# Kernel optimization log

Measured on AMD Instinct MI355X. Metric: run time of the kernel, lower is better.

The kernel has to match this reference:

```python
import jax, jax.numpy as jnp
import numpy as np

N_RULES = 4095
N_TAGS = N_RULES + 1
T = 1024
START = 0
NEG = -10000.0


def setup_inputs() -> dict:
    key = jax.random.key(0)
    k1, k2, k3 = jax.random.split(key, 3)
    feats = jax.random.normal(k1, (T, 1, N_RULES), dtype=jnp.float32)
    transitions = jax.random.normal(k2, (N_TAGS, N_TAGS), dtype=jnp.float32)
    transitions = transitions.at[START, :].set(NEG)  # matches nn.Parameter init edit
    tags = jax.random.randint(k3, (T,), 1, N_TAGS, dtype=jnp.int32)  # valid tags are 1..n_tags-1
    return {"feats": feats, "transitions": transitions, "tags": tags}


def reference(feats, transitions, tags):
    feats2 = feats[:, 0, :]  # [T, n_rules]

    # ---- log_cond_prob (score of the given tag path) ----
    tags_full = jnp.concatenate([jnp.array([START], dtype=tags.dtype), tags])  # [T+1]
    prev = tags_full[:-1]  # tags[t]   in torch code
    nxt = tags_full[1:]    # tags[t+1] in torch code
    # torch: feat[0][tags[t]-1]; tags[t]=0 gives index -1 (wraps) -> emulate with modulo
    emit = feats2[jnp.arange(T), (prev - 1) % N_RULES]          # [T]
    trans = transitions[nxt, prev]                               # [T]
    logprob = jnp.sum(emit + trans)

    # ---- log_normalizer (forward algorithm), vectorized over tags, scan over time ----
    init = jnp.full((N_TAGS,), NEG, dtype=feats.dtype).at[START].set(0.0)
    trans_tail = transitions[1:, :]  # [n_rules, n_tags]; row rule+1 of transitions
    neg_head = jnp.full((1,), NEG, dtype=feats.dtype)

    def step(acc, feat_t):
        # scores[rule, j] = acc[j] + feat_t[rule] + transitions[rule+1, j]
        scores = acc[None, :] + feat_t[:, None] + trans_tail     # [n_rules, n_tags]
        new_tail = jax.nn.logsumexp(scores, axis=1)              # [n_rules]
        new_acc = jnp.concatenate([neg_head, new_tail])          # acc[0] stays -10000
        return new_acc, None

    acc, _ = jax.lax.scan(step, init, feats2)
    Z = jax.nn.logsumexp(acc)

    return jnp.reshape(-(logprob - Z), (1,))
```

## Files before the change

kernel.cpp:

```cpp
#include <hip/hip_runtime.h>


#define T_STEPS 1024
#define NRULES  4095
#define NTAGS   4096
#define RING    8
#define L2E     1.4426950408889634f
#define LN2     0.69314718055994530942

__device__ __forceinline__ float ld_agent(const float* p) {
  return __hip_atomic_load(p, __ATOMIC_RELAXED, __HIP_MEMORY_SCOPE_AGENT);
}
__device__ __forceinline__ void st_agent(float* p, float v) {
  __hip_atomic_store(p, v, __ATOMIC_RELAXED, __HIP_MEMORY_SCOPE_AGENT);
}

__global__ void crf_init(float* __restrict__ pring) {
  const float NANF = __builtin_nanf("");
  int idx = blockIdx.x * blockDim.x + threadIdx.x;
  int stride = gridDim.x * blockDim.x;
  for (int i = idx; i < RING * NTAGS; i += stride) {
    int slot = i >> 12;
    float v = (slot == 0) ? ((i == 0) ? 1.0f : 0.0f) : NANF;
    st_agent(&pring[i], v);
  }
}

__global__ void crf_logprob(const float* __restrict__ feats,
                            const float* __restrict__ trans,
                            const int* __restrict__ tags,
                            float* __restrict__ lp) {
  int t = threadIdx.x;
  int prev = (t == 0) ? 0 : tags[t - 1];
  int nxt  = tags[t];
  int er = prev - 1; if (er < 0) er += NRULES;
  float v = feats[(size_t)t * NRULES + er] + trans[(size_t)nxt * NTAGS + prev];
  #pragma unroll
  for (int d = 32; d; d >>= 1) v += __shfl_xor(v, d, 64);
  __shared__ float sb[16];
  if ((t & 63) == 0) sb[t >> 6] = v;
  __syncthreads();
  if (t == 0) {
    float s = 0.f;
    #pragma unroll
    for (int i = 0; i < 16; ++i) s += sb[i];
    lp[0] = s;
  }
}

__launch_bounds__(512, 2)
__global__ void crf_scan(const float* __restrict__ feats,
                         const float* __restrict__ trans,
                         float* __restrict__ pring,
                         const float* __restrict__ lp,
                         float* __restrict__ out)
{
  const int g    = blockIdx.x;
  const int tid  = threadIdx.x;
  const int wave = tid >> 6;
  const int lane = tid & 63;
  const int tagbase = g * 16 + wave * 2;

  __shared__ __align__(16) float stage[4352];
  __shared__ float wmax[8];
  __shared__ int giveup;

  float E0[64], E1[64];
  {
    const float* rp0 = trans + (size_t)(tagbase + 0) * NTAGS + lane * 64;
    const float* rp1 = trans + (size_t)(tagbase + 1) * NTAGS + lane * 64;
#define LDE(R, K) do {                                                  \
    const float4 v_ = *reinterpret_cast<const float4*>(rp##R + 4*(K));  \
    E##R[4*(K)+0] = __builtin_amdgcn_exp2f(v_.x * L2E);                 \
    E##R[4*(K)+1] = __builtin_amdgcn_exp2f(v_.y * L2E);                 \
    E##R[4*(K)+2] = __builtin_amdgcn_exp2f(v_.z * L2E);                 \
    E##R[4*(K)+3] = __builtin_amdgcn_exp2f(v_.w * L2E);                 \
  } while (0)
    LDE(0,0);  LDE(0,1);  LDE(0,2);  LDE(0,3);
    LDE(0,4);  LDE(0,5);  LDE(0,6);  LDE(0,7);
    LDE(0,8);  LDE(0,9);  LDE(0,10); LDE(0,11);
    LDE(0,12); LDE(0,13); LDE(0,14); LDE(0,15);
    LDE(1,0);  LDE(1,1);  LDE(1,2);  LDE(1,3);
    LDE(1,4);  LDE(1,5);  LDE(1,6);  LDE(1,7);
    LDE(1,8);  LDE(1,9);  LDE(1,10); LDE(1,11);
    LDE(1,12); LDE(1,13); LDE(1,14); LDE(1,15);
#undef LDE
  }

  if (tid == 0) giveup = 0;

  double Racc = 0.0;

  for (int t = 1; t <= T_STEPS; ++t) {
    const int sprev = (t - 1) & (RING - 1);
    const int scur  = t & (RING - 1);
    const float* pprev = pring + sprev * NTAGS;

    __syncthreads();

    if (giveup) break;

    float pv[8];
    #pragma unroll
    for (int i = 0; i < 8; ++i) pv[i] = ld_agent(&pprev[tid + 512 * i]);
    {
      int rounds = 0;
      for (;;) {
        bool bad = false;
        #pragma unroll
        for (int i = 0; i < 8; ++i) bad |= (pv[i] != pv[i]);
        if (__ballot(bad) == 0ull) break;
        if (++rounds > (1 << 18)) { giveup = 1; break; }
        __builtin_amdgcn_s_sleep(1);
        #pragma unroll
        for (int i = 0; i < 8; ++i)
          if (pv[i] != pv[i]) pv[i] = ld_agent(&pprev[tid + 512 * i]);
      }
    }

    if (t >= 2 && wave == 0 && lane < 16)
      st_agent(&pring[((t - 2) & (RING - 1)) * NTAGS + g * 16 + lane],
               __builtin_nanf(""));

    float mloc = 0.0f;
    #pragma unroll
    for (int i = 0; i < 8; ++i) {
      const int f = tid + 512 * i;
      stage[f + 4 * (f >> 6)] = pv[i];
      mloc = fmaxf(mloc, pv[i]);
    }
    #pragma unroll
    for (int d = 32; d; d >>= 1) mloc = fmaxf(mloc, __shfl_xor(mloc, d, 64));
    if (lane == 0) wmax[wave] = mloc;

    const int fi0 = (tagbase == 0) ? 0 : tagbase - 1;
    const float fe0 = feats[(size_t)(t - 1) * NRULES + fi0] * L2E;
    const float fe1 = feats[(size_t)(t - 1) * NRULES + tagbase] * L2E;

    __syncthreads();

    if (giveup) break;

    float pmax = wmax[0];
    #pragma unroll
    for (int i = 1; i < 8; ++i) pmax = fmaxf(pmax, wmax[i]);
    const float rprev = __builtin_amdgcn_logf(pmax);
    Racc += (double)rprev;

    float a0 = 0.f, a1 = 0.f;
    const float* myp = stage + 68 * lane;
#define MAC4(K) do {                                                     \
    const float4 q_ = *reinterpret_cast<const float4*>(myp + 4*(K));     \
    a0 = fmaf(E0[4*(K)+0], q_.x, a0); a1 = fmaf(E1[4*(K)+0], q_.x, a1);  \
    a0 = fmaf(E0[4*(K)+1], q_.y, a0); a1 = fmaf(E1[4*(K)+1], q_.y, a1);  \
    a0 = fmaf(E0[4*(K)+2], q_.z, a0); a1 = fmaf(E1[4*(K)+2], q_.z, a1);  \
    a0 = fmaf(E0[4*(K)+3], q_.w, a0); a1 = fmaf(E1[4*(K)+3], q_.w, a1);  \
  } while (0)
    MAC4(0);  MAC4(1);  MAC4(2);  MAC4(3);
    MAC4(4);  MAC4(5);  MAC4(6);  MAC4(7);
    MAC4(8);  MAC4(9);  MAC4(10); MAC4(11);
    MAC4(12); MAC4(13); MAC4(14); MAC4(15);
#undef MAC4
    #pragma unroll
    for (int d = 32; d; d >>= 1) {
      a0 += __shfl_xor(a0, d, 64);
      a1 += __shfl_xor(a1, d, 64);
    }

    const float y0 = fe0 + __builtin_amdgcn_logf(a0) - rprev;
    const float y1 = fe1 + __builtin_amdgcn_logf(a1) - rprev;

    if (lane < 2) {
      const float y = (lane == 0) ? y0 : y1;
      st_agent(&pring[scur * NTAGS + tagbase + lane], __builtin_amdgcn_exp2f(y));
    }
  }

  if (g == 0) {
    const float* pT = pring + (T_STEPS & (RING - 1)) * NTAGS;
    float pv[8];
    #pragma unroll
    for (int i = 0; i < 8; ++i) pv[i] = ld_agent(&pT[tid + 512 * i]);
    {
      int rounds = 0;
      for (;;) {
        bool bad = false;
        #pragma unroll
        for (int i = 0; i < 8; ++i) bad |= (pv[i] != pv[i]);
        if (__ballot(bad) == 0ull) break;
        if (++rounds > (1 << 18)) break;
        __builtin_amdgcn_s_sleep(1);
        #pragma unroll
        for (int i = 0; i < 8; ++i)
          if (pv[i] != pv[i]) pv[i] = ld_agent(&pT[tid + 512 * i]);
      }
    }
    float s = 0.f;
    #pragma unroll
    for (int i = 0; i < 8; ++i) s += pv[i];
    #pragma unroll
    for (int d = 32; d; d >>= 1) s += __shfl_xor(s, d, 64);
    __syncthreads();
    if (lane == 0) wmax[wave] = s;
    __syncthreads();
    if (tid == 0) {
      float tot = 0.f;
      #pragma unroll
      for (int i = 0; i < 8; ++i) tot += wmax[i];
      const double Z2 = (double)__builtin_amdgcn_logf(tot) + Racc;
      out[0] = (float)(LN2 * Z2 - (double)lp[0]);
    }
  }
}

extern "C" void kernel_launch(void* const* d_in, const int* in_sizes, int n_in,
                              void* d_out, int out_size, void* d_ws, size_t ws_size,
                              hipStream_t stream) {
  const float* feats = (const float*)d_in[0];
  const float* trans = (const float*)d_in[1];
  const int*   tags  = (const int*)d_in[2];
  float* out   = (float*)d_out;
  float* pring = (float*)d_ws;
  float* lp    = pring + RING * NTAGS;

  crf_init<<<64, 256, 0, stream>>>(pring);
  crf_logprob<<<1, 1024, 0, stream>>>(feats, trans, tags, lp);
  crf_scan<<<256, 512, 0, stream>>>(feats, trans, pring, lp, out);
}
```

Before: 4.771 ms.

## Use per-block flags for step sync and fp16 exp-transitions in LDS with fdot2

Replaces the NaN-sentinel polling of the whole 4096-entry probability vector with per-block ready flags. One wave polls 256 flags using release/acquire ordering, then all threads read the vector once. The exponentiated transition rows move from registers into dynamic shared memory as packed fp16, and the normalized probabilities are also packed to fp16 so the inner product uses fdot2. This is meant to cut polling traffic, register pressure and FMA count per step, at the cost of fp16 precision, 136KB of LDS per block (which may drop occupancy from 2 blocks to 1 per CU), and an extra barrier per step.

```diff
diff --git a/kernel.cpp b/kernel.cpp
--- a/kernel.cpp
+++ b/kernel.cpp
@@ -8,6 +8,16 @@
 #define L2E     1.4426950408889634f
 #define LN2     0.69314718055994530942
 
+typedef __fp16 h2 __attribute__((ext_vector_type(2)));
+
+#if __has_builtin(__builtin_amdgcn_fdot2)
+#define FDOT2(a, b, c) __builtin_amdgcn_fdot2((a), (b), (c), false)
+#else
+__device__ __forceinline__ float FDOT2(h2 a, h2 b, float c) {
+  return c + (float)a[0] * (float)b[0] + (float)a[1] * (float)b[1];
+}
+#endif
+
 __device__ __forceinline__ float ld_agent(const float* p) {
   return __hip_atomic_load(p, __ATOMIC_RELAXED, __HIP_MEMORY_SCOPE_AGENT);
 }
@@ -15,15 +25,17 @@
   __hip_atomic_store(p, v, __ATOMIC_RELAXED, __HIP_MEMORY_SCOPE_AGENT);
 }
 
-__global__ void crf_init(float* __restrict__ pring) {
-  const float NANF = __builtin_nanf("");
+#define FLAGS_OFF (RING * NTAGS)
+#define LP_OFF    (FLAGS_OFF + RING * 256)
+
+__global__ void crf_init(float* __restrict__ ws) {
+  unsigned* flags = (unsigned*)(ws + FLAGS_OFF);
   int idx = blockIdx.x * blockDim.x + threadIdx.x;
   int stride = gridDim.x * blockDim.x;
-  for (int i = idx; i < RING * NTAGS; i += stride) {
-    int slot = i >> 12;
-    float v = (slot == 0) ? ((i == 0) ? 1.0f : 0.0f) : NANF;
-    st_agent(&pring[i], v);
-  }
+  for (int i = idx; i < NTAGS; i += stride)
+    ws[i] = (i == 0) ? 1.0f : 0.0f;
+  for (int i = idx; i < RING * 256; i += stride)
+    flags[i] = (i < 256) ? 1u : 0u;
 }
 
 __global__ void crf_logprob(const float* __restrict__ feats,
@@ -51,43 +63,38 @@
 __launch_bounds__(512, 2)
 __global__ void crf_scan(const float* __restrict__ feats,
                          const float* __restrict__ trans,
-                         float* __restrict__ pring,
-                         const float* __restrict__ lp,
+                         float* __restrict__ ws,
                          float* __restrict__ out)
 {
+  extern __shared__ __align__(16) char dynsm[];
+  char* const PS = dynsm + 131072;
+
+  float* const pring    = ws;
+  unsigned* const flags = (unsigned*)(ws + FLAGS_OFF);
+  const float* const lp = ws + LP_OFF;
+
   const int g    = blockIdx.x;
   const int tid  = threadIdx.x;
   const int wave = tid >> 6;
   const int lane = tid & 63;
-  const int tagbase = g * 16 + wave * 2;
-
-  __shared__ __align__(16) float stage[4352];
-  __shared__ float wmax[8];
+  const int tagbase = g * 16 + 2 * wave;
+
+  __shared__ float wmaxA[8];
   __shared__ int giveup;
-
-  float E0[64], E1[64];
+  if (tid == 0) giveup = 0;
+
   {
-    const float* rp0 = trans + (size_t)(tagbase + 0) * NTAGS + lane * 64;
-    const float* rp1 = trans + (size_t)(tagbase + 1) * NTAGS + lane * 64;
-#define LDE(R, K) do {                                                  \
-    const float4 v_ = *reinterpret_cast<const float4*>(rp##R + 4*(K));  \
-    E##R[4*(K)+0] = __builtin_amdgcn_exp2f(v_.x * L2E);                 \
-    E##R[4*(K)+1] = __builtin_amdgcn_exp2f(v_.y * L2E);                 \
-    E##R[4*(K)+2] = __builtin_amdgcn_exp2f(v_.z * L2E);                 \
-    E##R[4*(K)+3] = __builtin_amdgcn_exp2f(v_.w * L2E);                 \
-  } while (0)
-    LDE(0,0);  LDE(0,1);  LDE(0,2);  LDE(0,3);
-    LDE(0,4);  LDE(0,5);  LDE(0,6);  LDE(0,7);
-    LDE(0,8);  LDE(0,9);  LDE(0,10); LDE(0,11);
-    LDE(0,12); LDE(0,13); LDE(0,14); LDE(0,15);
-    LDE(1,0);  LDE(1,1);  LDE(1,2);  LDE(1,3);
-    LDE(1,4);  LDE(1,5);  LDE(1,6);  LDE(1,7);
-    LDE(1,8);  LDE(1,9);  LDE(1,10); LDE(1,11);
-    LDE(1,12); LDE(1,13); LDE(1,14); LDE(1,15);
-#undef LDE
-  }
-
-  if (tid == 0) giveup = 0;
+    const size_t base = (size_t)(g * 16) * NTAGS;
+    for (int i = tid; i < 16 * 2048; i += 512) {
+      const int row = i >> 11, pr = i & 2047;
+      const float2 v = *reinterpret_cast<const float2*>(
+          trans + base + (size_t)row * NTAGS + 2 * pr);
+      h2 e = __builtin_amdgcn_cvt_pkrtz(__builtin_amdgcn_exp2f(v.x * L2E),
+                                        __builtin_amdgcn_exp2f(v.y * L2E));
+      *reinterpret_cast<h2*>(dynsm + row * 8192 + 4 * pr) = e;
+    }
+  }
+  __syncthreads();
 
   double Racc = 0.0;
 
@@ -96,42 +103,37 @@
     const int scur  = t & (RING - 1);
     const float* pprev = pring + sprev * NTAGS;
 
-    __syncthreads();
-
-    if (giveup) break;
-
-    float pv[8];
-    #pragma unroll
-    for (int i = 0; i < 8; ++i) pv[i] = ld_agent(&pprev[tid + 512 * i]);
-    {
+    if (wave == 0) {
+      unsigned* fl = flags + sprev * 256;
       int rounds = 0;
       for (;;) {
-        bool bad = false;
-        #pragma unroll
-        for (int i = 0; i < 8; ++i) bad |= (pv[i] != pv[i]);
-        if (__ballot(bad) == 0ull) break;
-        if (++rounds > (1 << 18)) { giveup = 1; break; }
+        unsigned f0 = __hip_atomic_load(fl + lane,       __ATOMIC_RELAXED, __HIP_MEMORY_SCOPE_AGENT);
+        unsigned f1 = __hip_atomic_load(fl + lane + 64,  __ATOMIC_RELAXED, __HIP_MEMORY_SCOPE_AGENT);
+        unsigned f2 = __hip_atomic_load(fl + lane + 128, __ATOMIC_RELAXED, __HIP_MEMORY_SCOPE_AGENT);
+        unsigned f3 = __hip_atomic_load(fl + lane + 192, __ATOMIC_RELAXED, __HIP_MEMORY_SCOPE_AGENT);
+        bool ok = f0 && f1 && f2 && f3;
+        if (__ballot(!ok) == 0ull) break;
+        if (++rounds > (1 << 17)) { if (lane == 0) giveup = 1; break; }
         __builtin_amdgcn_s_sleep(1);
-        #pragma unroll
-        for (int i = 0; i < 8; ++i)
-          if (pv[i] != pv[i]) pv[i] = ld_agent(&pprev[tid + 512 * i]);
       }
-    }
-
-    if (t >= 2 && wave == 0 && lane < 16)
-      st_agent(&pring[((t - 2) & (RING - 1)) * NTAGS + g * 16 + lane],
-               __builtin_nanf(""));
-
+      (void)__hip_atomic_load(fl, __ATOMIC_ACQUIRE, __HIP_MEMORY_SCOPE_AGENT);
+    }
+    __syncthreads();
+    if (giveup) break;
+
+    if (t >= 2 && tid == 1)
+      __hip_atomic_store(&flags[((t - 2) & (RING - 1)) * 256 + g], 0u,
+                         __ATOMIC_RELAXED, __HIP_MEMORY_SCOPE_AGENT);
+
+    float pv[8];
+    #pragma unroll
+    for (int i = 0; i < 8; ++i) pv[i] = ld_agent(&pprev[8 * tid + i]);
     float mloc = 0.0f;
     #pragma unroll
-    for (int i = 0; i < 8; ++i) {
-      const int f = tid + 512 * i;
-      stage[f + 4 * (f >> 6)] = pv[i];
-      mloc = fmaxf(mloc, pv[i]);
-    }
+    for (int i = 0; i < 8; ++i) mloc = fmaxf(mloc, pv[i]);
     #pragma unroll
     for (int d = 32; d; d >>= 1) mloc = fmaxf(mloc, __shfl_xor(mloc, d, 64));
-    if (lane == 0) wmax[wave] = mloc;
+    if (lane == 0) wmaxA[wave] = mloc;
 
     const int fi0 = (tagbase == 0) ? 0 : tagbase - 1;
     const float fe0 = feats[(size_t)(t - 1) * NRULES + fi0] * L2E;
@@ -139,74 +141,94 @@
 
     __syncthreads();
 
-    if (giveup) break;
-
-    float pmax = wmax[0];
-    #pragma unroll
-    for (int i = 1; i < 8; ++i) pmax = fmaxf(pmax, wmax[i]);
+    float pmax = wmaxA[0];
+    #pragma unroll
+    for (int i = 1; i < 8; ++i) pmax = fmaxf(pmax, wmaxA[i]);
     const float rprev = __builtin_amdgcn_logf(pmax);
+    const float inv   = __builtin_amdgcn_rcpf(pmax);
     Racc += (double)rprev;
 
+    {
+      h2 q0 = __builtin_amdgcn_cvt_pkrtz(pv[0] * inv, pv[1] * inv);
+      h2 q1 = __builtin_amdgcn_cvt_pkrtz(pv[2] * inv, pv[3] * inv);
+      h2 q2 = __builtin_amdgcn_cvt_pkrtz(pv[4] * inv, pv[5] * inv);
+      h2 q3 = __builtin_amdgcn_cvt_pkrtz(pv[6] * inv, pv[7] * inv);
+      float4 qq;
+      qq.x = __builtin_bit_cast(float, q0);
+      qq.y = __builtin_bit_cast(float, q1);
+      qq.z = __builtin_bit_cast(float, q2);
+      qq.w = __builtin_bit_cast(float, q3);
+      *reinterpret_cast<float4*>(PS + 16 * tid) = qq;
+    }
+    __syncthreads();
+
     float a0 = 0.f, a1 = 0.f;
-    const float* myp = stage + 68 * lane;
-#define MAC4(K) do {                                                     \
-    const float4 q_ = *reinterpret_cast<const float4*>(myp + 4*(K));     \
-    a0 = fmaf(E0[4*(K)+0], q_.x, a0); a1 = fmaf(E1[4*(K)+0], q_.x, a1);  \
-    a0 = fmaf(E0[4*(K)+1], q_.y, a0); a1 = fmaf(E1[4*(K)+1], q_.y, a1);  \
-    a0 = fmaf(E0[4*(K)+2], q_.z, a0); a1 = fmaf(E1[4*(K)+2], q_.z, a1);  \
-    a0 = fmaf(E0[4*(K)+3], q_.w, a0); a1 = fmaf(E1[4*(K)+3], q_.w, a1);  \
-  } while (0)
-    MAC4(0);  MAC4(1);  MAC4(2);  MAC4(3);
-    MAC4(4);  MAC4(5);  MAC4(6);  MAC4(7);
-    MAC4(8);  MAC4(9);  MAC4(10); MAC4(11);
-    MAC4(12); MAC4(13); MAC4(14); MAC4(15);
-#undef MAC4
+    const char* Er0 = dynsm + (2 * wave) * 8192;
+    const char* Er1 = Er0 + 8192;
+    #pragma unroll
+    for (int k = 0; k < 8; ++k) {
+      const int off = 1024 * k + 16 * lane;
+      const float4 pq = *reinterpret_cast<const float4*>(PS + off);
+      const float4 e0 = *reinterpret_cast<const float4*>(Er0 + off);
+      const float4 e1 = *reinterpret_cast<const float4*>(Er1 + off);
+      const h2 p0 = __builtin_bit_cast(h2, pq.x), p1 = __builtin_bit_cast(h2, pq.y);
+      const h2 p2 = __builtin_bit_cast(h2, pq.z), p3 = __builtin_bit_cast(h2, pq.w);
+      a0 = FDOT2(__builtin_bit_cast(h2, e0.x), p0, a0);
+      a0 = FDOT2(__builtin_bit_cast(h2, e0.y), p1, a0);
+      a0 = FDOT2(__builtin_bit_cast(h2, e0.z), p2, a0);
+      a0 = FDOT2(__builtin_bit_cast(h2, e0.w), p3, a0);
+      a1 = FDOT2(__builtin_bit_cast(h2, e1.x), p0, a1);
+      a1 = FDOT2(__builtin_bit_cast(h2, e1.y), p1, a1);
+      a1 = FDOT2(__builtin_bit_cast(h2, e1.z), p2, a1);
+      a1 = FDOT2(__builtin_bit_cast(h2, e1.w), p3, a1);
+    }
     #pragma unroll
     for (int d = 32; d; d >>= 1) {
       a0 += __shfl_xor(a0, d, 64);
       a1 += __shfl_xor(a1, d, 64);
     }
 
-    const float y0 = fe0 + __builtin_amdgcn_logf(a0) - rprev;
-    const float y1 = fe1 + __builtin_amdgcn_logf(a1) - rprev;
-
     if (lane < 2) {
-      const float y = (lane == 0) ? y0 : y1;
+      const float y = (lane == 0) ? (fe0 + __builtin_amdgcn_logf(a0))
+                                  : (fe1 + __builtin_amdgcn_logf(a1));
       st_agent(&pring[scur * NTAGS + tagbase + lane], __builtin_amdgcn_exp2f(y));
     }
-  }
-
-  if (g == 0) {
-    const float* pT = pring + (T_STEPS & (RING - 1)) * NTAGS;
-    float pv[8];
-    #pragma unroll
-    for (int i = 0; i < 8; ++i) pv[i] = ld_agent(&pT[tid + 512 * i]);
-    {
+    __syncthreads();
+    if (tid == 0)
+      __hip_atomic_store(&flags[scur * 256 + g], 1u,
+                         __ATOMIC_RELEASE, __HIP_MEMORY_SCOPE_AGENT);
+  }
+
+  if (g == 0 && !giveup) {
+    const int sT = T_STEPS & (RING - 1);
+    if (wave == 0) {
+      unsigned* fl = flags + sT * 256;
       int rounds = 0;
       for (;;) {
-        bool bad = false;
-        #pragma unroll
-        for (int i = 0; i < 8; ++i) bad |= (pv[i] != pv[i]);
-        if (__ballot(bad) == 0ull) break;
-        if (++rounds > (1 << 18)) break;
+        unsigned f0 = __hip_atomic_load(fl + lane,       __ATOMIC_RELAXED, __HIP_MEMORY_SCOPE_AGENT);
+        unsigned f1 = __hip_atomic_load(fl + lane + 64,  __ATOMIC_RELAXED, __HIP_MEMORY_SCOPE_AGENT);
+        unsigned f2 = __hip_atomic_load(fl + lane + 128, __ATOMIC_RELAXED, __HIP_MEMORY_SCOPE_AGENT);
+        unsigned f3 = __hip_atomic_load(fl + lane + 192, __ATOMIC_RELAXED, __HIP_MEMORY_SCOPE_AGENT);
+        bool ok = f0 && f1 && f2 && f3;
+        if (__ballot(!ok) == 0ull) break;
+        if (++rounds > (1 << 17)) break;
         __builtin_amdgcn_s_sleep(1);
-        #pragma unroll
-        for (int i = 0; i < 8; ++i)
-          if (pv[i] != pv[i]) pv[i] = ld_agent(&pT[tid + 512 * i]);
       }
-    }
+      (void)__hip_atomic_load(fl, __ATOMIC_ACQUIRE, __HIP_MEMORY_SCOPE_AGENT);
+    }
+    __syncthreads();
+    const float* pT = pring + sT * NTAGS;
     float s = 0.f;
     #pragma unroll
-    for (int i = 0; i < 8; ++i) s += pv[i];
+    for (int i = 0; i < 8; ++i) s += ld_agent(&pT[8 * tid + i]);
     #pragma unroll
     for (int d = 32; d; d >>= 1) s += __shfl_xor(s, d, 64);
-    __syncthreads();
-    if (lane == 0) wmax[wave] = s;
+    if (lane == 0) wmaxA[wave] = s;
     __syncthreads();
     if (tid == 0) {
       float tot = 0.f;
       #pragma unroll
-      for (int i = 0; i < 8; ++i) tot += wmax[i];
+      for (int i = 0; i < 8; ++i) tot += wmaxA[i];
       const double Z2 = (double)__builtin_amdgcn_logf(tot) + Racc;
       out[0] = (float)(LN2 * Z2 - (double)lp[0]);
     }
@@ -219,11 +241,13 @@
   const float* feats = (const float*)d_in[0];
   const float* trans = (const float*)d_in[1];
   const int*   tags  = (const int*)d_in[2];
-  float* out   = (float*)d_out;
-  float* pring = (float*)d_ws;
-  float* lp    = pring + RING * NTAGS;
-
-  crf_init<<<64, 256, 0, stream>>>(pring);
-  crf_logprob<<<1, 1024, 0, stream>>>(feats, trans, tags, lp);
-  crf_scan<<<256, 512, 0, stream>>>(feats, trans, pring, lp, out);
-}
+  float* out = (float*)d_out;
+  float* ws  = (float*)d_ws;
+
+  (void)hipFuncSetAttribute(reinterpret_cast<const void*>(crf_scan),
+                            hipFuncAttributeMaxDynamicSharedMemorySize, 139264);
+
+  crf_init<<<64, 256, 0, stream>>>(ws);
+  crf_logprob<<<1, 1024, 0, stream>>>(feats, trans, tags, ws + LP_OFF);
+  crf_scan<<<256, 512, 139264, stream>>>(feats, trans, ws, out);
+}
```

Result: slower. 12.06 ms (+152.8%).
